# Kernel optimization log

Measured on AMD Instinct MI355X. Metric: run time of the kernel, lower is better.

## Reference

```python
import jax, jax.numpy as jnp
import numpy as np

N = 50000      # nodes
E = 800000     # edges (avg degree 16)
F_IN = 128
H = 128
C = 64


def _lin(k, fan_in, fan_out):
    bound = 1.0 / np.sqrt(fan_in)
    kw, kb = jax.random.split(k)
    W = jax.random.uniform(kw, (fan_in, fan_out), jnp.float32, -bound, bound)
    b = jax.random.uniform(kb, (fan_out,), jnp.float32, -bound, bound)
    return W, b


def setup_inputs() -> dict:
    key = jax.random.key(0)
    ks = jax.random.split(key, 8)
    W1, b1 = _lin(ks[3], F_IN, H)
    W2, b2 = _lin(ks[4], H, H)
    W3, b3 = _lin(ks[5], H, H)
    Wr, br = _lin(ks[6], F_IN, H)
    Wo, bo = _lin(ks[7], H, C)
    return {
        "x": jax.random.normal(ks[0], (N, F_IN), jnp.float32),
        "src": jax.random.randint(ks[1], (E,), 0, N, jnp.int32),
        "dst": jax.random.randint(ks[2], (E,), 0, N, jnp.int32),
        "W1": W1, "b1": b1,
        "W2": W2, "b2": b2,
        "W3": W3, "b3": b3,
        "Wr": Wr, "br": br,
        "Wo": Wo, "bo": bo,
    }


def _degree_norms(src, dst, n):
    ones = jnp.ones(src.shape[0], jnp.float32)
    deg_out = jax.ops.segment_sum(ones, src, num_segments=n)
    deg_in = jax.ops.segment_sum(ones, dst, num_segments=n)
    # DGL norm='both': clamp zero-degree to 1 to avoid inf
    d_src = jnp.where(deg_out > 0, deg_out, 1.0) ** -0.5
    d_dst = jnp.where(deg_in > 0, deg_in, 1.0) ** -0.5
    return d_src, d_dst


def _graph_conv(x, W, b, src, dst, d_src, d_dst, n):
    # h = D_dst^{-1/2} A D_src^{-1/2} (x W) + b
    h = (x * d_src[:, None]) @ W              # [N, out]
    agg = jax.ops.segment_sum(h[src], dst, num_segments=n)  # SpMM via gather/scatter
    return agg * d_dst[:, None] + b


def reference(x, src, dst, W1, b1, W2, b2, W3, b3, Wr, br, Wo, bo):
    n = x.shape[0]
    d_src, d_dst = _degree_norms(src, dst, n)
    res = x @ Wr + br
    out = jax.nn.relu(_graph_conv(x, W1, b1, src, dst, d_src, d_dst, n))
    out = jax.nn.relu(_graph_conv(out, W2, b2, src, dst, d_src, d_dst, n))
    out = _graph_conv(out, W3, b3, src, dst, d_src, d_dst, n)
    out = jax.nn.relu(out + res)
    return out @ Wo + bo
```

## Files before the change

### kernel.cpp

```cpp
#include <hip/hip_runtime.h>
#include <cstdint>
#include <cstddef>

#define FD 128
#define CO 64
#define NB 256
#define NBINS 256

typedef short bf16x8 __attribute__((ext_vector_type(8)));
typedef float f32x4 __attribute__((ext_vector_type(4)));
typedef unsigned int uint32;
typedef unsigned char uint8;
typedef unsigned short ushort;

__device__ __forceinline__ ushort f2bf(float f) {
  unsigned u = __float_as_uint(f);
  unsigned r = u + 0x7fffu + ((u >> 16) & 1u);
  return (ushort)(r >> 16);
}
__device__ __forceinline__ float bf2f(ushort b) {
  return __uint_as_float((unsigned)b << 16);
}


__global__ __launch_bounds__(256) void k_hist(const int* __restrict__ src,
                                              const int* __restrict__ dst,
                                              int* __restrict__ histD,
                                              int* __restrict__ histS,
                                              int E, int chunk) {
  __shared__ int hd[NBINS], hs[NBINS];
  int tid = threadIdx.x, blk = blockIdx.x;
  hd[tid] = 0;
  hs[tid] = 0;
  __syncthreads();
  int beg = blk * chunk;
  int end = min(E, beg + chunk);
  for (int e = beg + tid; e < end; e += 256) {
    atomicAdd(&hd[dst[e] >> 8], 1);
    atomicAdd(&hs[src[e] >> 8], 1);
  }
  __syncthreads();
  histD[tid * NB + blk] = hd[tid];
  histS[tid * NB + blk] = hs[tid];
}

__global__ __launch_bounds__(256) void k_ssum(int* __restrict__ a,
                                              int* __restrict__ b,
                                              int* __restrict__ bsums) {
  const int* p = blockIdx.y ? b : a;
  __shared__ int red[256];
  int tid = threadIdx.x;
  red[tid] = p[blockIdx.x * 256 + tid];
  __syncthreads();
  for (int o = 128; o > 0; o >>= 1) {
    if (tid < o) red[tid] += red[tid + o];
    __syncthreads();
  }
  if (tid == 0) bsums[blockIdx.y * 256 + blockIdx.x] = red[0];
}

__global__ __launch_bounds__(256) void k_sscan(int* __restrict__ bsums) {
  __shared__ int s[256];
  int tid = threadIdx.x;
  for (int r = 0; r < 2; r++) {
    int v = bsums[r * 256 + tid];
    s[tid] = v;
    __syncthreads();
    for (int o = 1; o < 256; o <<= 1) {
      int t = (tid >= o) ? s[tid - o] : 0;
      __syncthreads();
      s[tid] += t;
      __syncthreads();
    }
    bsums[r * 256 + tid] = s[tid] - v;
    __syncthreads();
  }
}

__global__ __launch_bounds__(256) void k_sapply(int* __restrict__ a,
                                                int* __restrict__ b,
                                                const int* __restrict__ bsums) {
  int* p = blockIdx.y ? b : a;
  int boff = bsums[blockIdx.y * 256 + blockIdx.x];
  __shared__ int s[256];
  int tid = threadIdx.x;
  int i = blockIdx.x * 256 + tid;
  int v = p[i];
  s[tid] = v;
  __syncthreads();
  for (int o = 1; o < 256; o <<= 1) {
    int t = (tid >= o) ? s[tid - o] : 0;
    __syncthreads();
    s[tid] += t;
    __syncthreads();
  }
  p[i] = boff + s[tid] - v;
}

__global__ __launch_bounds__(256) void k_scatter(const int* __restrict__ src,
                                                 const int* __restrict__ dst,
                                                 const int* __restrict__ offD,
                                                 const int* __restrict__ offS,
                                                 uint32* __restrict__ pk,
                                                 uint8* __restrict__ srcS8,
                                                 int E, int chunk) {
  __shared__ int runD[NBINS], runS[NBINS];
  int tid = threadIdx.x, blk = blockIdx.x;
  runD[tid] = offD[tid * NB + blk];
  runS[tid] = offS[tid * NB + blk];
  __syncthreads();
  int beg = blk * chunk;
  int end = min(E, beg + chunk);
  for (int e = beg + tid; e < end; e += 256) {
    int s = src[e], d = dst[e];
    int p = atomicAdd(&runD[d >> 8], 1);
    pk[p] = ((uint32)s << 8) | (uint32)(d & 255);
    int q = atomicAdd(&runS[s >> 8], 1);
    srcS8[q] = (uint8)(s & 255);
  }
}

__global__ __launch_bounds__(256) void k_bucket_dst(const uint32* __restrict__ pk,
                                                    const int* __restrict__ offD,
                                                    ushort* __restrict__ esrc,
                                                    int* __restrict__ row_ptr,
                                                    float* __restrict__ d_dst,
                                                    int N, int E) {
  __shared__ int cnt[NBINS], run[NBINS];
  int tid = threadIdx.x, bin = blockIdx.x;
  int start = offD[bin * NB];
  int end = (bin == NBINS - 1) ? E : offD[(bin + 1) * NB];
  cnt[tid] = 0;
  __syncthreads();
  for (int p = start + tid; p < end; p += 256) atomicAdd(&cnt[pk[p] & 255], 1);
  __syncthreads();
  int v = cnt[tid];
  run[tid] = v;
  __syncthreads();
  for (int o = 1; o < 256; o <<= 1) {
    int t = (tid >= o) ? run[tid - o] : 0;
    __syncthreads();
    run[tid] += t;
    __syncthreads();
  }
  int excl = run[tid] - v;
  int node = bin * 256 + tid;
  if (node < N) {
    row_ptr[node] = start + excl;
    d_dst[node] = rsqrtf((float)(v > 0 ? v : 1));
  }
  __syncthreads();
  run[tid] = start + excl;
  __syncthreads();
  for (int p = start + tid; p < end; p += 256) {
    uint32 v2 = pk[p];
    int slot = atomicAdd(&run[v2 & 255], 1);
    esrc[slot] = (ushort)(v2 >> 8);
  }
  if (bin == 0 && tid == 0) row_ptr[N] = E;
}

__global__ __launch_bounds__(256) void k_bucket_src(const uint8* __restrict__ srcS8,
                                                    const int* __restrict__ offS,
                                                    float* __restrict__ d_src,
                                                    int N, int E) {
  __shared__ int cnt[NBINS];
  int tid = threadIdx.x, bin = blockIdx.x;
  int start = offS[bin * NB];
  int end = (bin == NBINS - 1) ? E : offS[(bin + 1) * NB];
  cnt[tid] = 0;
  __syncthreads();
  for (int p = start + tid; p < end; p += 256) atomicAdd(&cnt[srcS8[p]], 1);
  __syncthreads();
  int node = bin * 256 + tid;
  if (node < N) {
    int v = cnt[tid];
    d_src[node] = rsqrtf((float)(v > 0 ? v : 1));
  }
}


__global__ __launch_bounds__(256) void k_wsplit(const float* __restrict__ W1,
                                                const float* __restrict__ W2,
                                                const float* __restrict__ W3,
                                                const float* __restrict__ Wr,
                                                const float* __restrict__ Wo,
                                                bf16x8* __restrict__ Whg,
                                                bf16x8* __restrict__ Wlg) {
  int idx = blockIdx.x * 256 + threadIdx.x;
  if (idx >= 9216) return;
  int region = idx >> 11;
  if (idx >= 8192) region = 4;
  const float* W = (region == 0) ? W1 : (region == 1) ? W2 : (region == 2) ? W3
                   : (region == 3) ? Wr : Wo;
  int cols = (region < 4) ? FD : CO;
  int local = idx - region * 2048;
  int kc = local / cols, col = local - kc * cols;
  bf16x8 h, l;
#pragma unroll
  for (int j = 0; j < 8; j++) {
    float v = W[(size_t)(kc * 8 + j) * cols + col];
    ushort hb = f2bf(v);
    h[j] = (short)hb;
    l[j] = (short)f2bf(v - bf2f(hb));
  }
  Whg[idx] = h;
  Wlg[idx] = l;
}


__global__ __launch_bounds__(256) void k_gemm_dual(const float* __restrict__ x,
                                                   const bf16x8* __restrict__ Wh1,
                                                   const bf16x8* __restrict__ Wl1,
                                                   const float* __restrict__ d_src,
                                                   const bf16x8* __restrict__ Whr,
                                                   const bf16x8* __restrict__ Wlr,
                                                   const float* __restrict__ br,
                                                   ushort* __restrict__ out1,
                                                   ushort* __restrict__ out2,
                                                   int N) {
  __shared__ bf16x8 Ah[1024];
  int tid = threadIdx.x;
  int rowBase = blockIdx.x * 64;

#pragma unroll
  for (int t = 0; t < 4; t++) {
    int p = t * 256 + tid;
    int kc = p >> 6, row = p & 63;
    int gr = rowBase + row;
    bf16x8 h = {0, 0, 0, 0, 0, 0, 0, 0};
    if (gr < N) {
      const float4* A4 = (const float4*)(x + (size_t)gr * FD + kc * 8);
      float4 u = A4[0];
      float4 v = A4[1];
      float vals[8] = {u.x, u.y, u.z, u.w, v.x, v.y, v.z, v.w};
#pragma unroll
      for (int j = 0; j < 8; j++) h[j] = (short)f2bf(vals[j]);
    }
    Ah[kc * 64 + row] = h;
  }
  __syncthreads();

  int wv = tid >> 6, lane = tid & 63;
  int wr = (wv >> 1) * 32;
  int wc = (wv & 1) * 64;
  int lhi = lane >> 4, llo = lane & 15;

#pragma unroll
  for (int pass = 0; pass < 2; pass++) {
    const bf16x8* Wh = pass ? Whr : Wh1;
    const bf16x8* Wl = pass ? Wlr : Wl1;
    f32x4 acc[2][4] = {};
#pragma unroll
    for (int ks = 0; ks < 4; ks++) {
      int kcg = ks * 4 + lhi;
      int abase = kcg * 64 + wr + llo;
      bf16x8 a0 = Ah[abase];
      bf16x8 a1 = Ah[abase + 16];
      int bbase = kcg * FD + wc + llo;
#pragma unroll
      for (int nf = 0; nf < 4; nf++) {
        bf16x8 bh = Wh[bbase + nf * 16];
        bf16x8 bl = Wl[bbase + nf * 16];
        acc[0][nf] = __builtin_amdgcn_mfma_f32_16x16x32_bf16(a0, bh, acc[0][nf], 0, 0, 0);
        acc[1][nf] = __builtin_amdgcn_mfma_f32_16x16x32_bf16(a1, bh, acc[1][nf], 0, 0, 0);
        acc[0][nf] = __builtin_amdgcn_mfma_f32_16x16x32_bf16(a0, bl, acc[0][nf], 0, 0, 0);
        acc[1][nf] = __builtin_amdgcn_mfma_f32_16x16x32_bf16(a1, bl, acc[1][nf], 0, 0, 0);
      }
    }
#pragma unroll
    for (int nf = 0; nf < 4; nf++) {
      int col = wc + nf * 16 + llo;
      float bv = pass ? br[col] : 0.f;
#pragma unroll
      for (int mf = 0; mf < 2; mf++) {
#pragma unroll
        for (int r = 0; r < 4; r++) {
          int row = rowBase + wr + mf * 16 + lhi * 4 + r;
          if (row < N) {
            float v = acc[mf][nf][r];
            if (pass == 0) v *= d_src[row];
            else v += bv;
            ushort* o = pass ? out2 : out1;
            o[(size_t)row * FD + col] = f2bf(v);
          }
        }
      }
    }
  }
}


template <int NCW, bool RES, bool NEXTSCALE, bool BIASOUT, bool OUTBF16>
__global__ __launch_bounds__(1024) void k_aggemm(const ushort* __restrict__ h,
                                                 const int* __restrict__ row_ptr,
                                                 const ushort* __restrict__ esrc,
                                                 const float* __restrict__ d_dst,
                                                 const float* __restrict__ bias_in,
                                                 const float* __restrict__ d_src,
                                                 const ushort* __restrict__ res,
                                                 const bf16x8* __restrict__ Wh,
                                                 const bf16x8* __restrict__ Wl,
                                                 const float* __restrict__ bias_out,
                                                 void* __restrict__ outv, int N) {
  constexpr int NF = NCW / 64;
  __shared__ bf16x8 Alds[1024];
  int tid = threadIdx.x;
  int wv = tid >> 6, lane = tid & 63;
  int rowBase = blockIdx.x * 64;
  int sub = lane >> 4, sl = lane & 15;
  int r = wv * 4 + sub;
  int gr = rowBase + r;
  const uint4* h16 = (const uint4*)h;

  float4 bA = ((const float4*)bias_in)[sl * 2];
  float4 bB = ((const float4*)bias_in)[sl * 2 + 1];
  float bia[8] = {bA.x, bA.y, bA.z, bA.w, bB.x, bB.y, bB.z, bB.w};

  float val[8];
#pragma unroll
  for (int j = 0; j < 8; j++) val[j] = 0.f;

  if (gr < N) {
    int beg = row_ptr[gr], end = row_ptr[gr + 1];
    float a[8] = {0.f, 0.f, 0.f, 0.f, 0.f, 0.f, 0.f, 0.f};
    int e = beg;
    for (; e + 16 <= end; e += 16) {
      int s[16];
#pragma unroll
      for (int j = 0; j < 16; j++) s[j] = esrc[e + j];
      uint4 v[16];
#pragma unroll
      for (int j = 0; j < 16; j++) v[j] = h16[(size_t)s[j] * 16 + sl];
#pragma unroll
      for (int j = 0; j < 16; j++) {
        a[0] += bf2f((ushort)(v[j].x & 0xffff));
        a[1] += bf2f((ushort)(v[j].x >> 16));
        a[2] += bf2f((ushort)(v[j].y & 0xffff));
        a[3] += bf2f((ushort)(v[j].y >> 16));
        a[4] += bf2f((ushort)(v[j].z & 0xffff));
        a[5] += bf2f((ushort)(v[j].z >> 16));
        a[6] += bf2f((ushort)(v[j].w & 0xffff));
        a[7] += bf2f((ushort)(v[j].w >> 16));
      }
    }
    if (e < end) {
      int cnt = end - e;
      int s[16];
#pragma unroll
      for (int j = 0; j < 16; j++) s[j] = (j < cnt) ? (int)esrc[e + j] : 0;
      uint4 v[16];
#pragma unroll
      for (int j = 0; j < 16; j++)
        if (j < cnt) v[j] = h16[(size_t)s[j] * 16 + sl];
#pragma unroll
      for (int j = 0; j < 16; j++) {
        if (j < cnt) {
          a[0] += bf2f((ushort)(v[j].x & 0xffff));
          a[1] += bf2f((ushort)(v[j].x >> 16));
          a[2] += bf2f((ushort)(v[j].y & 0xffff));
          a[3] += bf2f((ushort)(v[j].y >> 16));
          a[4] += bf2f((ushort)(v[j].z & 0xffff));
          a[5] += bf2f((ushort)(v[j].z >> 16));
          a[6] += bf2f((ushort)(v[j].w & 0xffff));
          a[7] += bf2f((ushort)(v[j].w >> 16));
        }
      }
    }
    float d = d_dst[gr];
#pragma unroll
    for (int j = 0; j < 8; j++) val[j] = a[j] * d + bia[j];
    if (RES) {
      uint4 rv = ((const uint4*)res)[(size_t)gr * 16 + sl];
      val[0] += bf2f((ushort)(rv.x & 0xffff));
      val[1] += bf2f((ushort)(rv.x >> 16));
      val[2] += bf2f((ushort)(rv.y & 0xffff));
      val[3] += bf2f((ushort)(rv.y >> 16));
      val[4] += bf2f((ushort)(rv.z & 0xffff));
      val[5] += bf2f((ushort)(rv.z >> 16));
      val[6] += bf2f((ushort)(rv.w & 0xffff));
      val[7] += bf2f((ushort)(rv.w >> 16));
    }
#pragma unroll
    for (int j = 0; j < 8; j++) val[j] = fmaxf(val[j], 0.f);
    if (NEXTSCALE) {
      float sc = d_src[gr];
#pragma unroll
      for (int j = 0; j < 8; j++) val[j] *= sc;
    }
  }
  bf16x8 o;
#pragma unroll
  for (int j = 0; j < 8; j++) o[j] = (short)f2bf(val[j]);
  Alds[r * 16 + (sl ^ (r & 7))] = o;
  __syncthreads();

  int wr = (wv >> 2) * 16;
  int wc = (wv & 3) * (NCW / 4);
  int lhi = lane >> 4, llo = lane & 15;
  f32x4 acc[NF] = {};

#pragma unroll
  for (int ks = 0; ks < 4; ks++) {
    int kcg = ks * 4 + lhi;
    int row0 = wr + llo;
    bf16x8 a0 = Alds[row0 * 16 + (kcg ^ (row0 & 7))];
    int bbase = kcg * NCW + wc + llo;
#pragma unroll
    for (int nf = 0; nf < NF; nf++) {
      bf16x8 bh = Wh[bbase + nf * 16];
      bf16x8 bl = Wl[bbase + nf * 16];
      acc[nf] = __builtin_amdgcn_mfma_f32_16x16x32_bf16(a0, bh, acc[nf], 0, 0, 0);
      acc[nf] = __builtin_amdgcn_mfma_f32_16x16x32_bf16(a0, bl, acc[nf], 0, 0, 0);
    }
  }

#pragma unroll
  for (int nf = 0; nf < NF; nf++) {
    int col = wc + nf * 16 + llo;
    float bv = BIASOUT ? bias_out[col] : 0.f;
#pragma unroll
    for (int rr = 0; rr < 4; rr++) {
      int row = rowBase + wr + lhi * 4 + rr;
      if (row < N) {
        float v = acc[nf][rr] + bv;
        if (OUTBF16)
          ((ushort*)outv)[(size_t)row * NCW + col] = f2bf(v);
        else
          ((float*)outv)[(size_t)row * NCW + col] = v;
      }
    }
  }
}


extern "C" void kernel_launch(void* const* d_in, const int* in_sizes, int n_in,
                              void* d_out, int out_size, void* d_ws, size_t ws_size,
                              hipStream_t stream) {
  (void)n_in; (void)out_size; (void)ws_size;
  const float* x  = (const float*)d_in[0];
  const int*   src = (const int*)d_in[1];
  const int*   dst = (const int*)d_in[2];
  const float* W1 = (const float*)d_in[3];
  const float* b1 = (const float*)d_in[4];
  const float* W2 = (const float*)d_in[5];
  const float* b2 = (const float*)d_in[6];
  const float* W3 = (const float*)d_in[7];
  const float* b3 = (const float*)d_in[8];
  const float* Wr = (const float*)d_in[9];
  const float* br = (const float*)d_in[10];
  const float* Wo = (const float*)d_in[11];
  const float* bo = (const float*)d_in[12];
  float* out = (float*)d_out;

  const int N = in_sizes[0] / FD;
  const int E = in_sizes[1];

  char* ws = (char*)d_ws;
  size_t off = 0;
  auto alloc = [&](size_t bytes) -> void* {
    void* p = ws + off;
    off += (bytes + 255) & ~size_t(255);
    return p;
  };
  int* histD   = (int*)alloc((size_t)NBINS * NB * 4);
  int* histS   = (int*)alloc((size_t)NBINS * NB * 4);
  int* bsums   = (int*)alloc(2 * 256 * 4);
  uint32* pk   = (uint32*)alloc((size_t)E * 4);
  uint8* srcS8 = (uint8*)alloc((size_t)E);
  ushort* esrc = (ushort*)alloc((size_t)E * 2);
  int* row_ptr = (int*)alloc((size_t)(N + 1) * 4);
  float* d_src = (float*)alloc((size_t)N * 4);
  float* d_dst = (float*)alloc((size_t)N * 4);
  bf16x8* Whg  = (bf16x8*)alloc(9216 * 16);
  bf16x8* Wlg  = (bf16x8*)alloc(9216 * 16);
  ushort* tb0  = (ushort*)alloc((size_t)N * FD * 2);
  ushort* tb1  = (ushort*)alloc((size_t)N * FD * 2);
  ushort* resb = (ushort*)alloc((size_t)N * FD * 2);

  int chunk = (E + NB - 1) / NB;
  dim3 gScan(256, 2);

  k_wsplit<<<36, 256, 0, stream>>>(W1, W2, W3, Wr, Wo, Whg, Wlg);
  k_hist<<<NB, 256, 0, stream>>>(src, dst, histD, histS, E, chunk);
  k_ssum<<<gScan, 256, 0, stream>>>(histD, histS, bsums);
  k_sscan<<<1, 256, 0, stream>>>(bsums);
  k_sapply<<<gScan, 256, 0, stream>>>(histD, histS, bsums);
  k_scatter<<<NB, 256, 0, stream>>>(src, dst, histD, histS, pk, srcS8, E, chunk);
  k_bucket_dst<<<NBINS, 256, 0, stream>>>(pk, histD, esrc, row_ptr, d_dst, N, E);
  k_bucket_src<<<NBINS, 256, 0, stream>>>(srcS8, histS, d_src, N, E);

  int gG = (N + 63) / 64;

  const bf16x8* Wh1 = Whg;
  const bf16x8* Wh2 = Whg + 2048;
  const bf16x8* Wh3 = Whg + 4096;
  const bf16x8* Whr = Whg + 6144;
  const bf16x8* Who = Whg + 8192;
  const bf16x8* Wl1 = Wlg;
  const bf16x8* Wl2 = Wlg + 2048;
  const bf16x8* Wl3 = Wlg + 4096;
  const bf16x8* Wlr = Wlg + 6144;
  const bf16x8* Wlo = Wlg + 8192;

  k_gemm_dual<<<gG, 256, 0, stream>>>(x, Wh1, Wl1, d_src, Whr, Wlr, br, tb0, resb, N);
  k_aggemm<FD, false, true, false, true><<<gG, 1024, 0, stream>>>(
      tb0, row_ptr, esrc, d_dst, b1, d_src, nullptr, Wh2, Wl2, nullptr, tb1, N);
  k_aggemm<FD, false, true, false, true><<<gG, 1024, 0, stream>>>(
      tb1, row_ptr, esrc, d_dst, b2, d_src, nullptr, Wh3, Wl3, nullptr, tb0, N);
  k_aggemm<CO, true, false, true, false><<<gG, 1024, 0, stream>>>(
      tb0, row_ptr, esrc, d_dst, b3, nullptr, resb, Who, Wlo, bo, out, N);
}
```

Baseline: 221.2 us.

## Merge bucket kernels and halve aggemm block size with two rows per sub-wave

The two bucketing kernels are fused into one launch that uses blockIdx.y to pick the dst or src path, removing a launch. The aggregation+GEMM kernel now runs with 512 threads per block. Each quarter-wave handles two destination rows in sequence, and each wave computes two 16-row MFMA tiles. The gather unroll drops from 16 to 8 with a scalar tail loop, which cuts register pressure but exposes less memory-level parallelism per row.

```diff
diff --git a/kernel.cpp b/kernel.cpp
--- a/kernel.cpp
+++ b/kernel.cpp
@@ -120,62 +120,60 @@
   }
 }
 
-__global__ __launch_bounds__(256) void k_bucket_dst(const uint32* __restrict__ pk,
-                                                    const int* __restrict__ offD,
-                                                    ushort* __restrict__ esrc,
-                                                    int* __restrict__ row_ptr,
-                                                    float* __restrict__ d_dst,
-                                                    int N, int E) {
+__global__ __launch_bounds__(256) void k_bucket(const uint32* __restrict__ pk,
+                                                const int* __restrict__ offD,
+                                                const uint8* __restrict__ srcS8,
+                                                const int* __restrict__ offS,
+                                                ushort* __restrict__ esrc,
+                                                int* __restrict__ row_ptr,
+                                                float* __restrict__ d_dst,
+                                                float* __restrict__ d_src,
+                                                int N, int E) {
   __shared__ int cnt[NBINS], run[NBINS];
   int tid = threadIdx.x, bin = blockIdx.x;
-  int start = offD[bin * NB];
-  int end = (bin == NBINS - 1) ? E : offD[(bin + 1) * NB];
-  cnt[tid] = 0;
-  __syncthreads();
-  for (int p = start + tid; p < end; p += 256) atomicAdd(&cnt[pk[p] & 255], 1);
-  __syncthreads();
-  int v = cnt[tid];
-  run[tid] = v;
-  __syncthreads();
-  for (int o = 1; o < 256; o <<= 1) {
-    int t = (tid >= o) ? run[tid - o] : 0;
-    __syncthreads();
-    run[tid] += t;
-    __syncthreads();
-  }
-  int excl = run[tid] - v;
-  int node = bin * 256 + tid;
-  if (node < N) {
-    row_ptr[node] = start + excl;
-    d_dst[node] = rsqrtf((float)(v > 0 ? v : 1));
-  }
-  __syncthreads();
-  run[tid] = start + excl;
-  __syncthreads();
-  for (int p = start + tid; p < end; p += 256) {
-    uint32 v2 = pk[p];
-    int slot = atomicAdd(&run[v2 & 255], 1);
-    esrc[slot] = (ushort)(v2 >> 8);
-  }
-  if (bin == 0 && tid == 0) row_ptr[N] = E;
-}
-
-__global__ __launch_bounds__(256) void k_bucket_src(const uint8* __restrict__ srcS8,
-                                                    const int* __restrict__ offS,
-                                                    float* __restrict__ d_src,
-                                                    int N, int E) {
-  __shared__ int cnt[NBINS];
-  int tid = threadIdx.x, bin = blockIdx.x;
-  int start = offS[bin * NB];
-  int end = (bin == NBINS - 1) ? E : offS[(bin + 1) * NB];
-  cnt[tid] = 0;
-  __syncthreads();
-  for (int p = start + tid; p < end; p += 256) atomicAdd(&cnt[srcS8[p]], 1);
-  __syncthreads();
-  int node = bin * 256 + tid;
-  if (node < N) {
+  if (blockIdx.y == 0) {
+    int start = offD[bin * NB];
+    int end = (bin == NBINS - 1) ? E : offD[(bin + 1) * NB];
+    cnt[tid] = 0;
+    __syncthreads();
+    for (int p = start + tid; p < end; p += 256) atomicAdd(&cnt[pk[p] & 255], 1);
+    __syncthreads();
     int v = cnt[tid];
-    d_src[node] = rsqrtf((float)(v > 0 ? v : 1));
+    run[tid] = v;
+    __syncthreads();
+    for (int o = 1; o < 256; o <<= 1) {
+      int t = (tid >= o) ? run[tid - o] : 0;
+      __syncthreads();
+      run[tid] += t;
+      __syncthreads();
+    }
+    int excl = run[tid] - v;
+    int node = bin * 256 + tid;
+    if (node < N) {
+      row_ptr[node] = start + excl;
+      d_dst[node] = rsqrtf((float)(v > 0 ? v : 1));
+    }
+    __syncthreads();
+    run[tid] = start + excl;
+    __syncthreads();
+    for (int p = start + tid; p < end; p += 256) {
+      uint32 v2 = pk[p];
+      int slot = atomicAdd(&run[v2 & 255], 1);
+      esrc[slot] = (ushort)(v2 >> 8);
+    }
+    if (bin == 0 && tid == 0) row_ptr[N] = E;
+  } else {
+    int start = offS[bin * NB];
+    int end = (bin == NBINS - 1) ? E : offS[(bin + 1) * NB];
+    cnt[tid] = 0;
+    __syncthreads();
+    for (int p = start + tid; p < end; p += 256) atomicAdd(&cnt[srcS8[p]], 1);
+    __syncthreads();
+    int node = bin * 256 + tid;
+    if (node < N) {
+      int v = cnt[tid];
+      d_src[node] = rsqrtf((float)(v > 0 ? v : 1));
+    }
   }
 }
 
@@ -292,70 +290,46 @@
 
 
 template <int NCW, bool RES, bool NEXTSCALE, bool BIASOUT, bool OUTBF16>
-__global__ __launch_bounds__(1024) void k_aggemm(const ushort* __restrict__ h,
-                                                 const int* __restrict__ row_ptr,
-                                                 const ushort* __restrict__ esrc,
-                                                 const float* __restrict__ d_dst,
-                                                 const float* __restrict__ bias_in,
-                                                 const float* __restrict__ d_src,
-                                                 const ushort* __restrict__ res,
-                                                 const bf16x8* __restrict__ Wh,
-                                                 const bf16x8* __restrict__ Wl,
-                                                 const float* __restrict__ bias_out,
-                                                 void* __restrict__ outv, int N) {
+__global__ __launch_bounds__(512) void k_aggemm(const ushort* __restrict__ h,
+                                                const int* __restrict__ row_ptr,
+                                                const ushort* __restrict__ esrc,
+                                                const float* __restrict__ d_dst,
+                                                const float* __restrict__ bias_in,
+                                                const float* __restrict__ d_src,
+                                                const ushort* __restrict__ res,
+                                                const bf16x8* __restrict__ Wh,
+                                                const bf16x8* __restrict__ Wl,
+                                                const float* __restrict__ bias_out,
+                                                void* __restrict__ outv, int N) {
   constexpr int NF = NCW / 64;
   __shared__ bf16x8 Alds[1024];
   int tid = threadIdx.x;
   int wv = tid >> 6, lane = tid & 63;
   int rowBase = blockIdx.x * 64;
   int sub = lane >> 4, sl = lane & 15;
-  int r = wv * 4 + sub;
-  int gr = rowBase + r;
   const uint4* h16 = (const uint4*)h;
 
   float4 bA = ((const float4*)bias_in)[sl * 2];
   float4 bB = ((const float4*)bias_in)[sl * 2 + 1];
   float bia[8] = {bA.x, bA.y, bA.z, bA.w, bB.x, bB.y, bB.z, bB.w};
 
-  float val[8];
-#pragma unroll
-  for (int j = 0; j < 8; j++) val[j] = 0.f;
-
-  if (gr < N) {
-    int beg = row_ptr[gr], end = row_ptr[gr + 1];
+  for (int rq = 0; rq < 2; rq++) {
+    int r = wv * 8 + rq * 4 + sub;
+    int gr = rowBase + r;
     float a[8] = {0.f, 0.f, 0.f, 0.f, 0.f, 0.f, 0.f, 0.f};
-    int e = beg;
-    for (; e + 16 <= end; e += 16) {
-      int s[16];
-#pragma unroll
-      for (int j = 0; j < 16; j++) s[j] = esrc[e + j];
-      uint4 v[16];
-#pragma unroll
-      for (int j = 0; j < 16; j++) v[j] = h16[(size_t)s[j] * 16 + sl];
-#pragma unroll
-      for (int j = 0; j < 16; j++) {
-        a[0] += bf2f((ushort)(v[j].x & 0xffff));
-        a[1] += bf2f((ushort)(v[j].x >> 16));
-        a[2] += bf2f((ushort)(v[j].y & 0xffff));
-        a[3] += bf2f((ushort)(v[j].y >> 16));
-        a[4] += bf2f((ushort)(v[j].z & 0xffff));
-        a[5] += bf2f((ushort)(v[j].z >> 16));
-        a[6] += bf2f((ushort)(v[j].w & 0xffff));
-        a[7] += bf2f((ushort)(v[j].w >> 16));
-      }
-    }
-    if (e < end) {
-      int cnt = end - e;
-      int s[16];
-#pragma unroll
-      for (int j = 0; j < 16; j++) s[j] = (j < cnt) ? (int)esrc[e + j] : 0;
-      uint4 v[16];
-#pragma unroll
-      for (int j = 0; j < 16; j++)
-        if (j < cnt) v[j] = h16[(size_t)s[j] * 16 + sl];
-#pragma unroll
-      for (int j = 0; j < 16; j++) {
-        if (j < cnt) {
+    float val[8];
+    if (gr < N) {
+      int beg = row_ptr[gr], end = row_ptr[gr + 1];
+      int e = beg;
+      for (; e + 8 <= end; e += 8) {
+        int s[8];
+#pragma unroll
+        for (int j = 0; j < 8; j++) s[j] = esrc[e + j];
+        uint4 v[8];
+#pragma unroll
+        for (int j = 0; j < 8; j++) v[j] = h16[(size_t)s[j] * 16 + sl];
+#pragma unroll
+        for (int j = 0; j < 8; j++) {
           a[0] += bf2f((ushort)(v[j].x & 0xffff));
           a[1] += bf2f((ushort)(v[j].x >> 16));
           a[2] += bf2f((ushort)(v[j].y & 0xffff));
@@ -366,52 +340,70 @@
           a[7] += bf2f((ushort)(v[j].w >> 16));
         }
       }
-    }
-    float d = d_dst[gr];
-#pragma unroll
-    for (int j = 0; j < 8; j++) val[j] = a[j] * d + bia[j];
-    if (RES) {
-      uint4 rv = ((const uint4*)res)[(size_t)gr * 16 + sl];
-      val[0] += bf2f((ushort)(rv.x & 0xffff));
-      val[1] += bf2f((ushort)(rv.x >> 16));
-      val[2] += bf2f((ushort)(rv.y & 0xffff));
-      val[3] += bf2f((ushort)(rv.y >> 16));
-      val[4] += bf2f((ushort)(rv.z & 0xffff));
-      val[5] += bf2f((ushort)(rv.z >> 16));
-      val[6] += bf2f((ushort)(rv.w & 0xffff));
-      val[7] += bf2f((ushort)(rv.w >> 16));
-    }
-#pragma unroll
-    for (int j = 0; j < 8; j++) val[j] = fmaxf(val[j], 0.f);
-    if (NEXTSCALE) {
-      float sc = d_src[gr];
-#pragma unroll
-      for (int j = 0; j < 8; j++) val[j] *= sc;
-    }
-  }
-  bf16x8 o;
-#pragma unroll
-  for (int j = 0; j < 8; j++) o[j] = (short)f2bf(val[j]);
-  Alds[r * 16 + (sl ^ (r & 7))] = o;
-  __syncthreads();
-
-  int wr = (wv >> 2) * 16;
+      for (; e < end; e++) {
+        uint4 v = h16[(size_t)esrc[e] * 16 + sl];
+        a[0] += bf2f((ushort)(v.x & 0xffff));
+        a[1] += bf2f((ushort)(v.x >> 16));
+        a[2] += bf2f((ushort)(v.y & 0xffff));
+        a[3] += bf2f((ushort)(v.y >> 16));
+        a[4] += bf2f((ushort)(v.z & 0xffff));
+        a[5] += bf2f((ushort)(v.z >> 16));
+        a[6] += bf2f((ushort)(v.w & 0xffff));
+        a[7] += bf2f((ushort)(v.w >> 16));
+      }
+      float d = d_dst[gr];
+#pragma unroll
+      for (int j = 0; j < 8; j++) val[j] = a[j] * d + bia[j];
+      if (RES) {
+        uint4 rv = ((const uint4*)res)[(size_t)gr * 16 + sl];
+        val[0] += bf2f((ushort)(rv.x & 0xffff));
+        val[1] += bf2f((ushort)(rv.x >> 16));
+        val[2] += bf2f((ushort)(rv.y & 0xffff));
+        val[3] += bf2f((ushort)(rv.y >> 16));
+        val[4] += bf2f((ushort)(rv.z & 0xffff));
+        val[5] += bf2f((ushort)(rv.z >> 16));
+        val[6] += bf2f((ushort)(rv.w & 0xffff));
+        val[7] += bf2f((ushort)(rv.w >> 16));
+      }
+#pragma unroll
+      for (int j = 0; j < 8; j++) val[j] = fmaxf(val[j], 0.f);
+      if (NEXTSCALE) {
+        float sc = d_src[gr];
+#pragma unroll
+        for (int j = 0; j < 8; j++) val[j] *= sc;
+      }
+    } else {
+#pragma unroll
+      for (int j = 0; j < 8; j++) val[j] = 0.f;
+    }
+    bf16x8 o;
+#pragma unroll
+    for (int j = 0; j < 8; j++) o[j] = (short)f2bf(val[j]);
+    Alds[r * 16 + (sl ^ (r & 7))] = o;
+  }
+  __syncthreads();
+
+  int wr = (wv >> 2) * 32;
   int wc = (wv & 3) * (NCW / 4);
   int lhi = lane >> 4, llo = lane & 15;
-  f32x4 acc[NF] = {};
+  f32x4 acc[2][NF] = {};
 
 #pragma unroll
   for (int ks = 0; ks < 4; ks++) {
     int kcg = ks * 4 + lhi;
     int row0 = wr + llo;
+    int row1 = wr + 16 + llo;
     bf16x8 a0 = Alds[row0 * 16 + (kcg ^ (row0 & 7))];
+    bf16x8 a1 = Alds[row1 * 16 + (kcg ^ (row1 & 7))];
     int bbase = kcg * NCW + wc + llo;
 #pragma unroll
     for (int nf = 0; nf < NF; nf++) {
       bf16x8 bh = Wh[bbase + nf * 16];
       bf16x8 bl = Wl[bbase + nf * 16];
-      acc[nf] = __builtin_amdgcn_mfma_f32_16x16x32_bf16(a0, bh, acc[nf], 0, 0, 0);
-      acc[nf] = __builtin_amdgcn_mfma_f32_16x16x32_bf16(a0, bl, acc[nf], 0, 0, 0);
+      acc[0][nf] = __builtin_amdgcn_mfma_f32_16x16x32_bf16(a0, bh, acc[0][nf], 0, 0, 0);
+      acc[1][nf] = __builtin_amdgcn_mfma_f32_16x16x32_bf16(a1, bh, acc[1][nf], 0, 0, 0);
+      acc[0][nf] = __builtin_amdgcn_mfma_f32_16x16x32_bf16(a0, bl, acc[0][nf], 0, 0, 0);
+      acc[1][nf] = __builtin_amdgcn_mfma_f32_16x16x32_bf16(a1, bl, acc[1][nf], 0, 0, 0);
     }
   }
 
@@ -420,14 +412,17 @@
     int col = wc + nf * 16 + llo;
     float bv = BIASOUT ? bias_out[col] : 0.f;
 #pragma unroll
-    for (int rr = 0; rr < 4; rr++) {
-      int row = rowBase + wr + lhi * 4 + rr;
-      if (row < N) {
-        float v = acc[nf][rr] + bv;
-        if (OUTBF16)
-          ((ushort*)outv)[(size_t)row * NCW + col] = f2bf(v);
-        else
-          ((float*)outv)[(size_t)row * NCW + col] = v;
+    for (int mf = 0; mf < 2; mf++) {
+#pragma unroll
+      for (int r = 0; r < 4; r++) {
+        int row = rowBase + wr + mf * 16 + lhi * 4 + r;
+        if (row < N) {
+          float v = acc[mf][nf][r] + bv;
+          if (OUTBF16)
+            ((ushort*)outv)[(size_t)row * NCW + col] = f2bf(v);
+          else
+            ((float*)outv)[(size_t)row * NCW + col] = v;
+        }
       }
     }
   }
@@ -480,6 +475,7 @@
 
   int chunk = (E + NB - 1) / NB;
   dim3 gScan(256, 2);
+  dim3 gBucket(NBINS, 2);
 
   k_wsplit<<<36, 256, 0, stream>>>(W1, W2, W3, Wr, Wo, Whg, Wlg);
   k_hist<<<NB, 256, 0, stream>>>(src, dst, histD, histS, E, chunk);
@@ -487,8 +483,8 @@
   k_sscan<<<1, 256, 0, stream>>>(bsums);
   k_sapply<<<gScan, 256, 0, stream>>>(histD, histS, bsums);
   k_scatter<<<NB, 256, 0, stream>>>(src, dst, histD, histS, pk, srcS8, E, chunk);
-  k_bucket_dst<<<NBINS, 256, 0, stream>>>(pk, histD, esrc, row_ptr, d_dst, N, E);
-  k_bucket_src<<<NBINS, 256, 0, stream>>>(srcS8, histS, d_src, N, E);
+  k_bucket<<<gBucket, 256, 0, stream>>>(pk, histD, srcS8, histS, esrc, row_ptr,
+                                        d_dst, d_src, N, E);
 
   int gG = (N + 63) / 64;
 
@@ -504,10 +500,10 @@
   const bf16x8* Wlo = Wlg + 8192;
 
   k_gemm_dual<<<gG, 256, 0, stream>>>(x, Wh1, Wl1, d_src, Whr, Wlr, br, tb0, resb, N);
-  k_aggemm<FD, false, true, false, true><<<gG, 1024, 0, stream>>>(
+  k_aggemm<FD, false, true, false, true><<<gG, 512, 0, stream>>>(
       tb0, row_ptr, esrc, d_dst, b1, d_src, nullptr, Wh2, Wl2, nullptr, tb1, N);
-  k_aggemm<FD, false, true, false, true><<<gG, 1024, 0, stream>>>(
+  k_aggemm<FD, false, true, false, true><<<gG, 512, 0, stream>>>(
       tb1, row_ptr, esrc, d_dst, b2, d_src, nullptr, Wh3, Wl3, nullptr, tb0, N);
-  k_aggemm<CO, true, false, true, false><<<gG, 1024, 0, stream>>>(
+  k_aggemm<CO, true, false, true, false><<<gG, 512, 0, stream>>>(
       tb0, row_ptr, esrc, d_dst, b3, nullptr, resb, Who, Wlo, bo, out, N);
 }
```

New measurement: 203.3 us. 8.1% less time.
